# Kernel tuning notes

Hardware: AMD Instinct MI355X
Metric: run time of the kernel (lower is better)

The kernel has to match this reference:

```python
import jax, jax.numpy as jnp
import numpy as np

HIDDEN = 2048
INPUT = 128
BATCH = 2048


def setup_inputs() -> dict:
    key = jax.random.key(0)
    k = jax.random.split(key, 7)
    inp = {
        "input": jax.random.normal(k[0], (BATCH, INPUT), dtype=jnp.float32),
        "hx_real": jax.random.normal(k[1], (BATCH, HIDDEN), dtype=jnp.float32),
        "hx_imag": jax.random.normal(k[2], (BATCH, HIDDEN), dtype=jnp.float32),
        "W_unitary": jax.random.normal(k[3], (5 * HIDDEN, INPUT), dtype=jnp.float32) / np.sqrt(INPUT),
        "b_unitary": jax.random.normal(k[4], (5 * HIDDEN,), dtype=jnp.float32) * 0.01,
        "beta": jnp.zeros((HIDDEN,), dtype=jnp.float32),
        "permutation": jax.random.permutation(k[5], HIDDEN).astype(jnp.int32),
    }
    return inp


def _householder_apply(v, h):
    # (I - 2 v v^H) h = h - 2 v (v^H h); same math as materializing the matrix.
    proj = jnp.sum(jnp.conj(v) * h, axis=-1, keepdims=True)
    return h - 2.0 * v * proj


def reference(input, hx_real, hx_imag, W_unitary, b_unitary, beta, permutation):
    hx = hx_real + 1j * hx_imag  # (B, H) complex64
    up = input @ W_unitary.T + b_unitary  # (B, 5H)
    phases = jnp.exp(1j * up)  # complex64, unit modulus
    d1, d2, d3, r1, r2 = jnp.split(phases, 5, axis=-1)

    h = jnp.fft.fft(d1 * hx, axis=-1)
    h = _householder_apply(r1, h)
    h = jnp.fft.ifft(d2 * h[:, permutation], axis=-1)
    h = d3 * _householder_apply(r2, h)

    # ModReLU: relu(|z| + beta) * exp(1j * angle(z))
    mag = jnp.abs(h)
    new_mag = jax.nn.relu(mag + beta)
    h = new_mag * jnp.exp(1j * jnp.angle(h))
    return h
```

## Files before the change

kernel.cpp:

```cpp
#include <hip/hip_runtime.h>
#include <hip/hip_fp16.h>

#define HID 2048
#define FIVEH 10240
#define INP 128
#define BATCH 2048

typedef _Float16 half8 __attribute__((ext_vector_type(8)));
typedef float f32x4 __attribute__((ext_vector_type(4)));

__device__ __forceinline__ half8 cvt8(const float* p) {
  float4 a = *(const float4*)p;
  float4 b = *(const float4*)(p + 4);
  half8 h;
  h[0] = (_Float16)a.x; h[1] = (_Float16)a.y; h[2] = (_Float16)a.z; h[3] = (_Float16)a.w;
  h[4] = (_Float16)b.x; h[5] = (_Float16)b.y; h[6] = (_Float16)b.z; h[7] = (_Float16)b.w;
  return h;
}

#define WSTRIDE 136
__global__ __launch_bounds__(256) void gemm_up(const float* __restrict__ A,
                                               const float* __restrict__ W,
                                               const float* __restrict__ bias,
                                               _Float16* __restrict__ up16,
                                               int row0, int nrows) {
  __shared__ _Float16 Ws[128 * WSTRIDE];
  int tid = threadIdx.x, wave = tid >> 6, lane = tid & 63;
  int bx = blockIdx.x;
  int by = blockIdx.y;
  int nl = lane & 15, quad = lane >> 4;

  {
    const float* src = W + (size_t)(bx * 128) * INP;
#pragma unroll
    for (int it = 0; it < 8; ++it) {
      int n = (it * 256 + tid) * 8;
      int col = n >> 7, k = n & 127;
      *(half8*)(Ws + col * WSTRIDE + k) = cvt8(src + n);
    }
  }

  half8 af[2][4];
  int rowbase = row0 + by * 128 + wave * 32;
#pragma unroll
  for (int mt = 0; mt < 2; ++mt) {
    const float* ar = A + (size_t)(rowbase + mt * 16 + nl) * INP + quad * 8;
#pragma unroll
    for (int ks = 0; ks < 4; ++ks) af[mt][ks] = cvt8(ar + ks * 32);
  }
  __syncthreads();

  f32x4 acc[2][8];
#pragma unroll
  for (int nt = 0; nt < 8; ++nt) {
    half8 bf[4];
#pragma unroll
    for (int ks = 0; ks < 4; ++ks)
      bf[ks] = *(const half8*)(Ws + (nt * 16 + nl) * WSTRIDE + quad * 8 + ks * 32);
#pragma unroll
    for (int mt = 0; mt < 2; ++mt) {
      f32x4 a = {0.f, 0.f, 0.f, 0.f};
#pragma unroll
      for (int ks = 0; ks < 4; ++ks)
        a = __builtin_amdgcn_mfma_f32_16x16x32_f16(af[mt][ks], bf[ks], a, 0, 0, 0);
      acc[mt][nt] = a;
    }
  }
  __syncthreads();

#pragma unroll
  for (int nt = 0; nt < 8; ++nt) {
    float bv = bias[bx * 128 + nt * 16 + nl];
#pragma unroll
    for (int mt = 0; mt < 2; ++mt) {
      int rl = wave * 32 + mt * 16 + quad * 4;
#pragma unroll
      for (int r = 0; r < 4; ++r)
        Ws[(rl + r) * WSTRIDE + nt * 16 + nl] = (_Float16)(acc[mt][nt][r] + bv);
    }
  }
  __syncthreads();

#pragma unroll
  for (int it = 0; it < 8; ++it) {
    int v = it * 256 + tid;
    int r = v >> 4, c8 = (v & 15) * 8;
    *(half8*)(up16 + (size_t)(by * 128 + r) * FIVEH + bx * 128 + c8) =
        *(const half8*)(Ws + r * WSTRIDE + c8);
  }
}

__device__ __forceinline__ float2 h2ld(const __half2* p, int i) {
  return __half22float2(p[i]);
}
__device__ __forceinline__ void h2st(__half2* p, int i, float x, float y) {
  p[i] = __floats2half2_rn(x, y);
}

__device__ __forceinline__ void fft_head(const float2 v[8], __half2* dst, int tid, float sgn) {
  const float R2 = 0.70710678118654752f;
  float2 o[8];
  {
    float x0r = v[0].x + v[4].x, x0i = v[0].y + v[4].y;
    float x1r = v[1].x + v[5].x, x1i = v[1].y + v[5].y;
    float x2r = v[2].x + v[6].x, x2i = v[2].y + v[6].y;
    float x3r = v[3].x + v[7].x, x3i = v[3].y + v[7].y;
    float t0r = x0r + x2r, t0i = x0i + x2i, t1r = x0r - x2r, t1i = x0i - x2i;
    float t2r = x1r + x3r, t2i = x1i + x3i, t3r = x1r - x3r, t3i = x1i - x3i;
    o[0].x = t0r + t2r;       o[0].y = t0i + t2i;
    o[4].x = t0r - t2r;       o[4].y = t0i - t2i;
    o[2].x = t1r - sgn * t3i; o[2].y = t1i + sgn * t3r;
    o[6].x = t1r + sgn * t3i; o[6].y = t1i - sgn * t3r;
  }
  {
    float x0r = v[0].x - v[4].x, x0i = v[0].y - v[4].y;
    float x1r = v[1].x - v[5].x, x1i = v[1].y - v[5].y;
    float x2r = v[2].x - v[6].x, x2i = v[2].y - v[6].y;
    float x3r = v[3].x - v[7].x, x3i = v[3].y - v[7].y;
    float y1r = (x1r - sgn * x1i) * R2,  y1i = (sgn * x1r + x1i) * R2;
    float y2r = -sgn * x2i,              y2i = sgn * x2r;
    float y3r = -(x3r + sgn * x3i) * R2, y3i = (sgn * x3r - x3i) * R2;
    float t0r = x0r + y2r, t0i = x0i + y2i, t1r = x0r - y2r, t1i = x0i - y2i;
    float t2r = y1r + y3r, t2i = y1i + y3i, t3r = y1r - y3r, t3i = y1i - y3i;
    o[1].x = t0r + t2r;       o[1].y = t0i + t2i;
    o[5].x = t0r - t2r;       o[5].y = t0i - t2i;
    o[3].x = t1r - sgn * t3i; o[3].y = t1i + sgn * t3r;
    o[7].x = t1r + sgn * t3i; o[7].y = t1i - sgn * t3r;
  }
  __half2* base = dst + 8 * tid;
#pragma unroll
  for (int j = 0; j < 8; ++j) h2st(base, j, o[j].x, o[j].y);
}

template <int L>
__device__ __forceinline__ void fft_mid(const __half2* __restrict__ src,
                                        __half2* __restrict__ dst, int tid, float sgn) {
  static_assert(256 % L == 0, "twiddle hoist requires 256 % L == 0");
  const int k = tid & (L - 1);
  float s1, c1;
  __sincosf(sgn * (1.5707963267948966f / (float)L) * (float)k, &s1, &c1);
  float c2 = c1 * c1 - s1 * s1, s2 = 2.f * c1 * s1;
  float c3 = c1 * c2 - s1 * s2, s3 = c1 * s2 + s1 * c2;
#pragma unroll
  for (int t = 0; t < 2; ++t) {
    int i = tid + (t << 8);
    int base4 = ((i - k) << 2) + k;
    float2 x0 = h2ld(src, i),        x1 = h2ld(src, i + 512);
    float2 x2 = h2ld(src, i + 1024), x3 = h2ld(src, i + 1536);
    float y1r = x1.x * c1 - x1.y * s1, y1i = x1.x * s1 + x1.y * c1;
    float y2r = x2.x * c2 - x2.y * s2, y2i = x2.x * s2 + x2.y * c2;
    float y3r = x3.x * c3 - x3.y * s3, y3i = x3.x * s3 + x3.y * c3;
    float t0r = x0.x + y2r, t0i = x0.y + y2i;
    float t1r = x0.x - y2r, t1i = x0.y - y2i;
    float t2r = y1r + y3r, t2i = y1i + y3i;
    float t3r = y1r - y3r, t3i = y1i - y3i;
    h2st(dst, base4,         t0r + t2r, t0i + t2i);
    h2st(dst, base4 + 2 * L, t0r - t2r, t0i - t2i);
    h2st(dst, base4 + L,     t1r - sgn * t3i, t1i + sgn * t3r);
    h2st(dst, base4 + 3 * L, t1r + sgn * t3i, t1i - sgn * t3r);
  }
}

__device__ __forceinline__ void fft_tail(const __half2* __restrict__ src, float2 h[8],
                                         int tid, float sgn) {
#pragma unroll
  for (int t = 0; t < 2; ++t) {
    int i = tid + (t << 8);
    float s1, c1;
    __sincosf(sgn * (1.5707963267948966f / 512.f) * (float)i, &s1, &c1);
    float c2 = c1 * c1 - s1 * s1, s2 = 2.f * c1 * s1;
    float c3 = c1 * c2 - s1 * s2, s3 = c1 * s2 + s1 * c2;
    float2 x0 = h2ld(src, i),        x1 = h2ld(src, i + 512);
    float2 x2 = h2ld(src, i + 1024), x3 = h2ld(src, i + 1536);
    float y1r = x1.x * c1 - x1.y * s1, y1i = x1.x * s1 + x1.y * c1;
    float y2r = x2.x * c2 - x2.y * s2, y2i = x2.x * s2 + x2.y * c2;
    float y3r = x3.x * c3 - x3.y * s3, y3i = x3.x * s3 + x3.y * c3;
    float t0r = x0.x + y2r, t0i = x0.y + y2i;
    float t1r = x0.x - y2r, t1i = x0.y - y2i;
    float t2r = y1r + y3r, t2i = y1i + y3i;
    float t3r = y1r - y3r, t3i = y1i - y3i;
    h[t].x     = t0r + t2r;       h[t].y     = t0i + t2i;
    h[t + 4].x = t0r - t2r;       h[t + 4].y = t0i - t2i;
    h[t + 2].x = t1r - sgn * t3i; h[t + 2].y = t1i + sgn * t3r;
    h[t + 6].x = t1r + sgn * t3i; h[t + 6].y = t1i - sgn * t3r;
  }
}

__device__ __forceinline__ void block_reduce2(float& pr, float& pi,
                                              float* redr, float* redi, int tid) {
  for (int off = 32; off > 0; off >>= 1) {
    pr += __shfl_down(pr, off, 64);
    pi += __shfl_down(pi, off, 64);
  }
  if ((tid & 63) == 0) { redr[tid >> 6] = pr; redi[tid >> 6] = pi; }
  __syncthreads();
  pr = redr[0] + redr[1] + redr[2] + redr[3];
  pi = redi[0] + redi[1] + redi[2] + redi[3];
}

#define ROW_PIPELINE(UP)                                                        \
  float2 hreg[8];                                                               \
  {                                                                             \
    float2 v[8];                                                                \
    _Pragma("unroll") for (int e = 0; e < 8; ++e) {                             \
      int k = tid + (e << 8);                                                   \
      float sv, cv; __sincosf(UP(e, 0), &sv, &cv);                              \
      float hr = hxr[(size_t)b * HID + k];                                      \
      float hi = hxi[(size_t)b * HID + k];                                      \
      v[e].x = cv * hr - sv * hi; v[e].y = cv * hi + sv * hr;                   \
    }                                                                           \
    fft_head(v, sA, tid, -1.f);                                                 \
  }                                                                             \
  __syncthreads();                                                              \
  fft_mid<8>(sA, sB, tid, -1.f);   __syncthreads();                             \
  fft_mid<32>(sB, sA, tid, -1.f);  __syncthreads();                             \
  fft_mid<128>(sA, sB, tid, -1.f); __syncthreads();                             \
  fft_tail(sB, hreg, tid, -1.f);                                                \
  float cc[8], ss[8];                                                           \
  {                                                                             \
    float pr = 0.f, pi = 0.f;                                                   \
    _Pragma("unroll") for (int e = 0; e < 8; ++e) {                             \
      float sv, cv; __sincosf(UP(e, 3), &sv, &cv);                              \
      cc[e] = cv; ss[e] = sv;                                                   \
      pr += cv * hreg[e].x + sv * hreg[e].y;                                    \
      pi += cv * hreg[e].y - sv * hreg[e].x;                                    \
    }                                                                           \
    block_reduce2(pr, pi, redr, redi, tid);                                     \
    _Pragma("unroll") for (int e = 0; e < 8; ++e) {                             \
      int k = tid + (e << 8);                                                   \
      h2st(sA, k, hreg[e].x - 2.f * (cc[e] * pr - ss[e] * pi),                  \
                  hreg[e].y - 2.f * (cc[e] * pi + ss[e] * pr));                 \
    }                                                                           \
  }                                                                             \
  __syncthreads();                                                              \
  {                                                                             \
    const float invN = 1.0f / (float)HID;                                       \
    float2 v[8];                                                                \
    _Pragma("unroll") for (int e = 0; e < 8; ++e) {                             \
      int k = tid + (e << 8);                                                   \
      float sv, cv; __sincosf(UP(e, 1), &sv, &cv);                              \
      float2 hh = h2ld(sA, perm[k]);                                            \
      v[e].x = (cv * hh.x - sv * hh.y) * invN;                                  \
      v[e].y = (cv * hh.y + sv * hh.x) * invN;                                  \
    }                                                                           \
    fft_head(v, sB, tid, 1.f);                                                  \
  }                                                                             \
  __syncthreads();                                                              \
  fft_mid<8>(sB, sA, tid, 1.f);   __syncthreads();                              \
  fft_mid<32>(sA, sB, tid, 1.f);  __syncthreads();                              \
  fft_mid<128>(sB, sA, tid, 1.f); __syncthreads();                              \
  fft_tail(sA, hreg, tid, 1.f);                                                 \
  float prj_r, prj_i;                                                           \
  {                                                                             \
    float pr = 0.f, pi = 0.f;                                                   \
    _Pragma("unroll") for (int e = 0; e < 8; ++e) {                             \
      float sv, cv; __sincosf(UP(e, 4), &sv, &cv);                              \
      cc[e] = cv; ss[e] = sv;                                                   \
      pr += cv * hreg[e].x + sv * hreg[e].y;                                    \
      pi += cv * hreg[e].y - sv * hreg[e].x;                                    \
    }                                                                           \
    block_reduce2(pr, pi, redr + 4, redi + 4, tid);                             \
    prj_r = pr; prj_i = pi;                                                     \
  }                                                                             \
  _Pragma("unroll") for (int e = 0; e < 8; ++e) {                               \
    int k = tid + (e << 8);                                                     \
    float hr = hreg[e].x - 2.f * (cc[e] * prj_r - ss[e] * prj_i);               \
    float hi = hreg[e].y - 2.f * (cc[e] * prj_i + ss[e] * prj_r);               \
    float s3, c3; __sincosf(UP(e, 2), &s3, &c3);                                \
    float zr = c3 * hr - s3 * hi;                                               \
    float zi = c3 * hi + s3 * hr;                                               \
    float mag = sqrtf(zr * zr + zi * zi);                                       \
    float nm = mag + beta[k];                                                   \
    nm = nm > 0.f ? nm : 0.f;                                                   \
    float orr, oii;                                                             \
    if (mag > 0.f) { float sc = nm / mag; orr = zr * sc; oii = zi * sc; }       \
    else { orr = nm; oii = 0.f; }                                               \
    long m = (long)b * HID + k;                                                 \
    if (omode == 1) {                                                           \
      const long half = (long)BATCH * HID;                                      \
      if (half + m < out_size_l) { out[m] = orr; out[half + m] = oii; }         \
    } else if (omode == 0) {                                                    \
      if (2 * m + 1 < out_size_l) {                                             \
        float2 o; o.x = orr; o.y = oii;                                         \
        *(float2*)(out + 2 * m) = o;                                            \
      }                                                                         \
    } else {                                                                    \
      if (m < out_size_l) out[m] = orr;                                         \
    }                                                                           \
  }

__global__ __launch_bounds__(256, 4) void urnn_row(const _Float16* __restrict__ up16,
                                                   const float* __restrict__ hxr,
                                                   const float* __restrict__ hxi,
                                                   const float* __restrict__ beta,
                                                   const int* __restrict__ perm,
                                                   float* __restrict__ out,
                                                   int row0, long out_size_l, int omode) {
  __shared__ __half2 sA[HID], sB[HID];
  __shared__ float redr[8], redi[8];

  int tid = threadIdx.x;
  int b = row0 + blockIdx.x;
  const _Float16* uprow = up16 + (size_t)blockIdx.x * FIVEH;
#define UPG(e, s) ((float)uprow[(s) * HID + tid + ((e) << 8)])
  ROW_PIPELINE(UPG)
#undef UPG
}

__global__ __launch_bounds__(256) void urnn_fused(const float* __restrict__ A,
                                                  const float* __restrict__ W,
                                                  const float* __restrict__ bias,
                                                  const float* __restrict__ hxr,
                                                  const float* __restrict__ hxi,
                                                  const float* __restrict__ beta,
                                                  const int* __restrict__ perm,
                                                  float* __restrict__ out,
                                                  long out_size_l, int omode) {
  __shared__ __half2 sA[HID], sB[HID];
  __shared__ float redr[8], redi[8];
  __shared__ float4 xs4[INP / 4];

  int tid = threadIdx.x;
  int b = blockIdx.x;

  if (tid < INP / 4) xs4[tid] = ((const float4*)(A + (size_t)b * INP))[tid];
  __syncthreads();

  float upreg[40];
#pragma unroll
  for (int se = 0; se < 40; ++se) {
    int n = ((se >> 3) << 11) + ((se & 7) << 8) + tid;
    upreg[se] = bias[n];
  }
  for (int kb = 0; kb < 4; ++kb) {
    float4 xv[8];
#pragma unroll
    for (int j = 0; j < 8; ++j) xv[j] = xs4[kb * 8 + j];
#pragma unroll
    for (int se = 0; se < 40; ++se) {
      int n = ((se >> 3) << 11) + ((se & 7) << 8) + tid;
      const float4* wr = (const float4*)(W + (size_t)n * INP + (kb << 5));
      float a = 0.f;
#pragma unroll
      for (int j = 0; j < 8; ++j) {
        float4 wv = wr[j];
        a += xv[j].x * wv.x + xv[j].y * wv.y + xv[j].z * wv.z + xv[j].w * wv.w;
      }
      upreg[se] += a;
    }
  }
#define UPR(e, s) (upreg[(s) * 8 + (e)])
  ROW_PIPELINE(UPR)
#undef UPR
}

extern "C" void kernel_launch(void* const* d_in, const int* in_sizes, int n_in,
                              void* d_out, int out_size, void* d_ws, size_t ws_size,
                              hipStream_t stream) {
  const float* input   = (const float*)d_in[0];
  const float* hx_real = (const float*)d_in[1];
  const float* hx_imag = (const float*)d_in[2];
  const float* W       = (const float*)d_in[3];
  const float* bvec    = (const float*)d_in[4];
  const float* beta    = (const float*)d_in[5];
  const int*   perm    = (const int*)d_in[6];

  int omode;
  if (out_size == BATCH * HID) omode = 2;
  else if (out_size == 2 * BATCH * HID) omode = 1;
  else omode = 0;

  const size_t rowbytes = (size_t)FIVEH * sizeof(_Float16);
  long chunk = (long)(ws_size / rowbytes);
  if (chunk > BATCH) chunk = BATCH;
  chunk &= ~127L;

  if (chunk >= 128) {
    _Float16* up16 = (_Float16*)d_ws;
    for (long row0 = 0; row0 < BATCH; row0 += chunk) {
      int rows = (int)((row0 + chunk <= BATCH) ? chunk : (BATCH - row0));
      dim3 g(FIVEH / 128, rows / 128);
      gemm_up<<<g, 256, 0, stream>>>(input, W, bvec, up16, (int)row0, rows);
      urnn_row<<<rows, 256, 0, stream>>>(up16, hx_real, hx_imag, beta, perm,
                                         (float*)d_out, (int)row0, (long)out_size, omode);
    }
  } else {
    urnn_fused<<<BATCH, 256, 0, stream>>>(input, W, bvec, hx_real, hx_imag, beta, perm,
                                          (float*)d_out, (long)out_size, omode);
  }
}
```

Measured before the change: 144.4 us.

## Process two batch rows per block in the per-row FFT kernel

Replaces the one-row-per-block urnn_row kernel with urnn_row2, which handles two rows per 256-thread block using doubled shared buffers. FFT twiddle factors, the permutation indices and the tail twiddles are computed once per block and reused across both rows, and the two rows share barriers. This cuts redundant sincos and sync overhead per row, at the cost of twice the shared memory per block, a lower occupancy hint (launch bounds 2 instead of 4), and half as many blocks.

```diff
diff --git a/kernel.cpp b/kernel.cpp
--- a/kernel.cpp
+++ b/kernel.cpp
@@ -161,20 +161,64 @@
   }
 }
 
-__device__ __forceinline__ void fft_tail(const __half2* __restrict__ src, float2 h[8],
+template <int L>
+__device__ __forceinline__ void fft_mid2(const __half2 (*__restrict__ src)[HID],
+                                         __half2 (*__restrict__ dst)[HID],
                                          int tid, float sgn) {
+  static_assert(256 % L == 0, "twiddle hoist requires 256 % L == 0");
+  const int k = tid & (L - 1);
+  float s1, c1;
+  __sincosf(sgn * (1.5707963267948966f / (float)L) * (float)k, &s1, &c1);
+  float c2 = c1 * c1 - s1 * s1, s2 = 2.f * c1 * s1;
+  float c3 = c1 * c2 - s1 * s2, s3 = c1 * s2 + s1 * c2;
+#pragma unroll
+  for (int r = 0; r < 2; ++r) {
+#pragma unroll
+    for (int t = 0; t < 2; ++t) {
+      int i = tid + (t << 8);
+      int base4 = ((i - k) << 2) + k;
+      float2 x0 = h2ld(src[r], i),        x1 = h2ld(src[r], i + 512);
+      float2 x2 = h2ld(src[r], i + 1024), x3 = h2ld(src[r], i + 1536);
+      float y1r = x1.x * c1 - x1.y * s1, y1i = x1.x * s1 + x1.y * c1;
+      float y2r = x2.x * c2 - x2.y * s2, y2i = x2.x * s2 + x2.y * c2;
+      float y3r = x3.x * c3 - x3.y * s3, y3i = x3.x * s3 + x3.y * c3;
+      float t0r = x0.x + y2r, t0i = x0.y + y2i;
+      float t1r = x0.x - y2r, t1i = x0.y - y2i;
+      float t2r = y1r + y3r, t2i = y1i + y3i;
+      float t3r = y1r - y3r, t3i = y1i - y3i;
+      h2st(dst[r], base4,         t0r + t2r, t0i + t2i);
+      h2st(dst[r], base4 + 2 * L, t0r - t2r, t0i - t2i);
+      h2st(dst[r], base4 + L,     t1r - sgn * t3i, t1i + sgn * t3r);
+      h2st(dst[r], base4 + 3 * L, t1r + sgn * t3i, t1i - sgn * t3r);
+    }
+  }
+}
+
+struct TailTw { float c1[2], s1[2], c2[2], s2[2], c3[2], s3[2]; };
+__device__ __forceinline__ TailTw tail_tw(int tid, float sgn) {
+  TailTw w;
 #pragma unroll
   for (int t = 0; t < 2; ++t) {
     int i = tid + (t << 8);
     float s1, c1;
     __sincosf(sgn * (1.5707963267948966f / 512.f) * (float)i, &s1, &c1);
-    float c2 = c1 * c1 - s1 * s1, s2 = 2.f * c1 * s1;
-    float c3 = c1 * c2 - s1 * s2, s3 = c1 * s2 + s1 * c2;
+    w.c1[t] = c1; w.s1[t] = s1;
+    w.c2[t] = c1 * c1 - s1 * s1; w.s2[t] = 2.f * c1 * s1;
+    w.c3[t] = c1 * w.c2[t] - s1 * w.s2[t]; w.s3[t] = c1 * w.s2[t] + s1 * w.c2[t];
+  }
+  return w;
+}
+
+__device__ __forceinline__ void fft_tail_row(const __half2* __restrict__ src, float2 h[8],
+                                             int tid, float sgn, const TailTw& w) {
+#pragma unroll
+  for (int t = 0; t < 2; ++t) {
+    int i = tid + (t << 8);
     float2 x0 = h2ld(src, i),        x1 = h2ld(src, i + 512);
     float2 x2 = h2ld(src, i + 1024), x3 = h2ld(src, i + 1536);
-    float y1r = x1.x * c1 - x1.y * s1, y1i = x1.x * s1 + x1.y * c1;
-    float y2r = x2.x * c2 - x2.y * s2, y2i = x2.x * s2 + x2.y * c2;
-    float y3r = x3.x * c3 - x3.y * s3, y3i = x3.x * s3 + x3.y * c3;
+    float y1r = x1.x * w.c1[t] - x1.y * w.s1[t], y1i = x1.x * w.s1[t] + x1.y * w.c1[t];
+    float y2r = x2.x * w.c2[t] - x2.y * w.s2[t], y2i = x2.x * w.s2[t] + x2.y * w.c2[t];
+    float y3r = x3.x * w.c3[t] - x3.y * w.s3[t], y3i = x3.x * w.s3[t] + x3.y * w.c3[t];
     float t0r = x0.x + y2r, t0i = x0.y + y2i;
     float t1r = x0.x - y2r, t1i = x0.y - y2i;
     float t2r = y1r + y3r, t2i = y1i + y3i;
@@ -186,6 +230,12 @@
   }
 }
 
+__device__ __forceinline__ void fft_tail(const __half2* __restrict__ src, float2 h[8],
+                                         int tid, float sgn) {
+  TailTw w = tail_tw(tid, sgn);
+  fft_tail_row(src, h, tid, sgn, w);
+}
+
 __device__ __forceinline__ void block_reduce2(float& pr, float& pi,
                                               float* redr, float* redi, int tid) {
   for (int off = 32; off > 0; off >>= 1) {
@@ -196,6 +246,141 @@
   __syncthreads();
   pr = redr[0] + redr[1] + redr[2] + redr[3];
   pi = redi[0] + redi[1] + redi[2] + redi[3];
+}
+
+__global__ __launch_bounds__(256, 2) void urnn_row2(const _Float16* __restrict__ up16,
+                                                    const float* __restrict__ hxr,
+                                                    const float* __restrict__ hxi,
+                                                    const float* __restrict__ beta,
+                                                    const int* __restrict__ perm,
+                                                    float* __restrict__ out,
+                                                    int row0, long out_size_l, int omode) {
+  __shared__ __half2 sA[2][HID], sB[2][HID];
+  __shared__ float redr[16], redi[16];
+
+  int tid = threadIdx.x;
+  int rb = blockIdx.x * 2;
+  int b0 = row0 + rb;
+  const _Float16* up0 = up16 + (size_t)rb * FIVEH;
+
+#pragma unroll
+  for (int r = 0; r < 2; ++r) {
+    const _Float16* up = up0 + (size_t)r * FIVEH;
+    float2 v[8];
+#pragma unroll
+    for (int e = 0; e < 8; ++e) {
+      int k = tid + (e << 8);
+      float sv, cv; __sincosf((float)up[k], &sv, &cv);
+      float hr = hxr[(size_t)(b0 + r) * HID + k];
+      float hi = hxi[(size_t)(b0 + r) * HID + k];
+      v[e].x = cv * hr - sv * hi; v[e].y = cv * hi + sv * hr;
+    }
+    fft_head(v, sA[r], tid, -1.f);
+  }
+  __syncthreads();
+  fft_mid2<8>(sA, sB, tid, -1.f);   __syncthreads();
+  fft_mid2<32>(sB, sA, tid, -1.f);  __syncthreads();
+  fft_mid2<128>(sA, sB, tid, -1.f); __syncthreads();
+
+  {
+    TailTw w = tail_tw(tid, -1.f);
+#pragma unroll
+    for (int r = 0; r < 2; ++r) {
+      const _Float16* up = up0 + (size_t)r * FIVEH;
+      float2 hreg[8];
+      fft_tail_row(sB[r], hreg, tid, -1.f, w);
+      float cc[8], ss[8];
+      float pr = 0.f, pi = 0.f;
+#pragma unroll
+      for (int e = 0; e < 8; ++e) {
+        float sv, cv; __sincosf((float)up[3 * HID + tid + (e << 8)], &sv, &cv);
+        cc[e] = cv; ss[e] = sv;
+        pr += cv * hreg[e].x + sv * hreg[e].y;
+        pi += cv * hreg[e].y - sv * hreg[e].x;
+      }
+      block_reduce2(pr, pi, redr + 4 * r, redi + 4 * r, tid);
+#pragma unroll
+      for (int e = 0; e < 8; ++e) {
+        int k = tid + (e << 8);
+        h2st(sA[r], k, hreg[e].x - 2.f * (cc[e] * pr - ss[e] * pi),
+                       hreg[e].y - 2.f * (cc[e] * pi + ss[e] * pr));
+      }
+    }
+  }
+  __syncthreads();
+
+  {
+    int pk[8];
+#pragma unroll
+    for (int e = 0; e < 8; ++e) pk[e] = perm[tid + (e << 8)];
+    const float invN = 1.0f / (float)HID;
+#pragma unroll
+    for (int r = 0; r < 2; ++r) {
+      const _Float16* up = up0 + (size_t)r * FIVEH;
+      float2 v[8];
+#pragma unroll
+      for (int e = 0; e < 8; ++e) {
+        int k = tid + (e << 8);
+        float sv, cv; __sincosf((float)up[HID + k], &sv, &cv);
+        float2 hh = h2ld(sA[r], pk[e]);
+        v[e].x = (cv * hh.x - sv * hh.y) * invN;
+        v[e].y = (cv * hh.y + sv * hh.x) * invN;
+      }
+      fft_head(v, sB[r], tid, 1.f);
+    }
+  }
+  __syncthreads();
+  fft_mid2<8>(sB, sA, tid, 1.f);   __syncthreads();
+  fft_mid2<32>(sA, sB, tid, 1.f);  __syncthreads();
+  fft_mid2<128>(sB, sA, tid, 1.f); __syncthreads();
+
+  {
+    TailTw w = tail_tw(tid, 1.f);
+#pragma unroll
+    for (int r = 0; r < 2; ++r) {
+      const _Float16* up = up0 + (size_t)r * FIVEH;
+      long b = b0 + r;
+      float2 hreg[8];
+      fft_tail_row(sA[r], hreg, tid, 1.f, w);
+      float cc[8], ss[8];
+      float pr = 0.f, pi = 0.f;
+#pragma unroll
+      for (int e = 0; e < 8; ++e) {
+        float sv, cv; __sincosf((float)up[4 * HID + tid + (e << 8)], &sv, &cv);
+        cc[e] = cv; ss[e] = sv;
+        pr += cv * hreg[e].x + sv * hreg[e].y;
+        pi += cv * hreg[e].y - sv * hreg[e].x;
+      }
+      block_reduce2(pr, pi, redr + 8 + 4 * r, redi + 8 + 4 * r, tid);
+#pragma unroll
+      for (int e = 0; e < 8; ++e) {
+        int k = tid + (e << 8);
+        float hr = hreg[e].x - 2.f * (cc[e] * pr - ss[e] * pi);
+        float hi = hreg[e].y - 2.f * (cc[e] * pi + ss[e] * pr);
+        float s3, c3; __sincosf((float)up[2 * HID + k], &s3, &c3);
+        float zr = c3 * hr - s3 * hi;
+        float zi = c3 * hi + s3 * hr;
+        float mag = sqrtf(zr * zr + zi * zi);
+        float nm = mag + beta[k];
+        nm = nm > 0.f ? nm : 0.f;
+        float orr, oii;
+        if (mag > 0.f) { float sc = nm / mag; orr = zr * sc; oii = zi * sc; }
+        else { orr = nm; oii = 0.f; }
+        long m = b * HID + k;
+        if (omode == 1) {
+          const long half = (long)BATCH * HID;
+          if (half + m < out_size_l) { out[m] = orr; out[half + m] = oii; }
+        } else if (omode == 0) {
+          if (2 * m + 1 < out_size_l) {
+            float2 o; o.x = orr; o.y = oii;
+            *(float2*)(out + 2 * m) = o;
+          }
+        } else {
+          if (m < out_size_l) out[m] = orr;
+        }
+      }
+    }
+  }
 }
 
 #define ROW_PIPELINE(UP)                                                        \
@@ -289,24 +474,6 @@
     }                                                                           \
   }
 
-__global__ __launch_bounds__(256, 4) void urnn_row(const _Float16* __restrict__ up16,
-                                                   const float* __restrict__ hxr,
-                                                   const float* __restrict__ hxi,
-                                                   const float* __restrict__ beta,
-                                                   const int* __restrict__ perm,
-                                                   float* __restrict__ out,
-                                                   int row0, long out_size_l, int omode) {
-  __shared__ __half2 sA[HID], sB[HID];
-  __shared__ float redr[8], redi[8];
-
-  int tid = threadIdx.x;
-  int b = row0 + blockIdx.x;
-  const _Float16* uprow = up16 + (size_t)blockIdx.x * FIVEH;
-#define UPG(e, s) ((float)uprow[(s) * HID + tid + ((e) << 8)])
-  ROW_PIPELINE(UPG)
-#undef UPG
-}
-
 __global__ __launch_bounds__(256) void urnn_fused(const float* __restrict__ A,
                                                   const float* __restrict__ W,
                                                   const float* __restrict__ bias,
@@ -381,8 +548,8 @@
       int rows = (int)((row0 + chunk <= BATCH) ? chunk : (BATCH - row0));
       dim3 g(FIVEH / 128, rows / 128);
       gemm_up<<<g, 256, 0, stream>>>(input, W, bvec, up16, (int)row0, rows);
-      urnn_row<<<rows, 256, 0, stream>>>(up16, hx_real, hx_imag, beta, perm,
-                                         (float*)d_out, (int)row0, (long)out_size, omode);
+      urnn_row2<<<rows / 2, 256, 0, stream>>>(up16, hx_real, hx_imag, beta, perm,
+                                              (float*)d_out, (int)row0, (long)out_size, omode);
     }
   } else {
     urnn_fused<<<BATCH, 256, 0, stream>>>(input, W, bvec, hx_real, hx_imag, beta, perm,
```

New measurement: 152.6 us. 1.06x slower.

## Restructure FFT as radix-8 passes with fp32 shared-memory staging

Applied to the files above, without the earlier changes.

Replaces the radix-8 head plus three radix-4 middle passes with a radix-8 head, two radix-8 passes and the radix-4 tail, cutting the number of shared-memory round trips and barriers per FFT. Shared-memory buffers change from half2 to float2, which removes the fp16 conversions and improves accuracy. In exchange it doubles shared-memory use per block, which may reduce occupancy, and the radix-8 passes use more registers for twiddles.

```diff
diff --git a/kernel.cpp b/kernel.cpp
--- a/kernel.cpp
+++ b/kernel.cpp
@@ -90,79 +90,79 @@
   }
 }
 
-__device__ __forceinline__ float2 h2ld(const __half2* p, int i) {
-  return __half22float2(p[i]);
-}
-__device__ __forceinline__ void h2st(__half2* p, int i, float x, float y) {
-  p[i] = __floats2half2_rn(x, y);
-}
-
-__device__ __forceinline__ void fft_head(const float2 v[8], __half2* dst, int tid, float sgn) {
+__device__ __forceinline__ float2 cmulcs(float2 a, float c, float s) {
+  float2 r; r.x = a.x * c - a.y * s; r.y = a.x * s + a.y * c; return r;
+}
+
+__device__ __forceinline__ void dft8(const float2 y[8], float2 o[8], float sgn) {
   const float R2 = 0.70710678118654752f;
+  float ta0r = y[0].x + y[4].x, ta0i = y[0].y + y[4].y;
+  float ta1r = y[0].x - y[4].x, ta1i = y[0].y - y[4].y;
+  float ta2r = y[2].x + y[6].x, ta2i = y[2].y + y[6].y;
+  float ta3r = y[2].x - y[6].x, ta3i = y[2].y - y[6].y;
+  float E0r = ta0r + ta2r, E0i = ta0i + ta2i;
+  float E2r = ta0r - ta2r, E2i = ta0i - ta2i;
+  float E1r = ta1r - sgn * ta3i, E1i = ta1i + sgn * ta3r;
+  float E3r = ta1r + sgn * ta3i, E3i = ta1i - sgn * ta3r;
+  float tb0r = y[1].x + y[5].x, tb0i = y[1].y + y[5].y;
+  float tb1r = y[1].x - y[5].x, tb1i = y[1].y - y[5].y;
+  float tb2r = y[3].x + y[7].x, tb2i = y[3].y + y[7].y;
+  float tb3r = y[3].x - y[7].x, tb3i = y[3].y - y[7].y;
+  float O0r = tb0r + tb2r, O0i = tb0i + tb2i;
+  float O2r = tb0r - tb2r, O2i = tb0i - tb2i;
+  float O1r = tb1r - sgn * tb3i, O1i = tb1i + sgn * tb3r;
+  float O3r = tb1r + sgn * tb3i, O3i = tb1i - sgn * tb3r;
+  float p1r = R2 * (O1r - sgn * O1i), p1i = R2 * (O1i + sgn * O1r);
+  float p2r = -sgn * O2i,             p2i = sgn * O2r;
+  float p3r = -R2 * (O3r + sgn * O3i), p3i = R2 * (sgn * O3r - O3i);
+  o[0].x = E0r + O0r; o[0].y = E0i + O0i;
+  o[4].x = E0r - O0r; o[4].y = E0i - O0i;
+  o[1].x = E1r + p1r; o[1].y = E1i + p1i;
+  o[5].x = E1r - p1r; o[5].y = E1i - p1i;
+  o[2].x = E2r + p2r; o[2].y = E2i + p2i;
+  o[6].x = E2r - p2r; o[6].y = E2i - p2i;
+  o[3].x = E3r + p3r; o[3].y = E3i + p3i;
+  o[7].x = E3r - p3r; o[7].y = E3i - p3i;
+}
+
+__device__ __forceinline__ void fft8_head(const float2 v[8], float2* dst, int tid, float sgn) {
   float2 o[8];
-  {
-    float x0r = v[0].x + v[4].x, x0i = v[0].y + v[4].y;
-    float x1r = v[1].x + v[5].x, x1i = v[1].y + v[5].y;
-    float x2r = v[2].x + v[6].x, x2i = v[2].y + v[6].y;
-    float x3r = v[3].x + v[7].x, x3i = v[3].y + v[7].y;
-    float t0r = x0r + x2r, t0i = x0i + x2i, t1r = x0r - x2r, t1i = x0i - x2i;
-    float t2r = x1r + x3r, t2i = x1i + x3i, t3r = x1r - x3r, t3i = x1i - x3i;
-    o[0].x = t0r + t2r;       o[0].y = t0i + t2i;
-    o[4].x = t0r - t2r;       o[4].y = t0i - t2i;
-    o[2].x = t1r - sgn * t3i; o[2].y = t1i + sgn * t3r;
-    o[6].x = t1r + sgn * t3i; o[6].y = t1i - sgn * t3r;
-  }
-  {
-    float x0r = v[0].x - v[4].x, x0i = v[0].y - v[4].y;
-    float x1r = v[1].x - v[5].x, x1i = v[1].y - v[5].y;
-    float x2r = v[2].x - v[6].x, x2i = v[2].y - v[6].y;
-    float x3r = v[3].x - v[7].x, x3i = v[3].y - v[7].y;
-    float y1r = (x1r - sgn * x1i) * R2,  y1i = (sgn * x1r + x1i) * R2;
-    float y2r = -sgn * x2i,              y2i = sgn * x2r;
-    float y3r = -(x3r + sgn * x3i) * R2, y3i = (sgn * x3r - x3i) * R2;
-    float t0r = x0r + y2r, t0i = x0i + y2i, t1r = x0r - y2r, t1i = x0i - y2i;
-    float t2r = y1r + y3r, t2i = y1i + y3i, t3r = y1r - y3r, t3i = y1i - y3i;
-    o[1].x = t0r + t2r;       o[1].y = t0i + t2i;
-    o[5].x = t0r - t2r;       o[5].y = t0i - t2i;
-    o[3].x = t1r - sgn * t3i; o[3].y = t1i + sgn * t3r;
-    o[7].x = t1r + sgn * t3i; o[7].y = t1i - sgn * t3r;
-  }
-  __half2* base = dst + 8 * tid;
-#pragma unroll
-  for (int j = 0; j < 8; ++j) h2st(base, j, o[j].x, o[j].y);
+  dft8(v, o, sgn);
+  float2* base = dst + (tid << 3);
+#pragma unroll
+  for (int j = 0; j < 8; ++j) base[j] = o[j];
 }
 
 template <int L>
-__device__ __forceinline__ void fft_mid(const __half2* __restrict__ src,
-                                        __half2* __restrict__ dst, int tid, float sgn) {
-  static_assert(256 % L == 0, "twiddle hoist requires 256 % L == 0");
+__device__ __forceinline__ void fft8_pass(const float2* __restrict__ src,
+                                          float2* __restrict__ dst, int tid, float sgn) {
   const int k = tid & (L - 1);
   float s1, c1;
-  __sincosf(sgn * (1.5707963267948966f / (float)L) * (float)k, &s1, &c1);
-  float c2 = c1 * c1 - s1 * s1, s2 = 2.f * c1 * s1;
-  float c3 = c1 * c2 - s1 * s2, s3 = c1 * s2 + s1 * c2;
-#pragma unroll
-  for (int t = 0; t < 2; ++t) {
-    int i = tid + (t << 8);
-    int base4 = ((i - k) << 2) + k;
-    float2 x0 = h2ld(src, i),        x1 = h2ld(src, i + 512);
-    float2 x2 = h2ld(src, i + 1024), x3 = h2ld(src, i + 1536);
-    float y1r = x1.x * c1 - x1.y * s1, y1i = x1.x * s1 + x1.y * c1;
-    float y2r = x2.x * c2 - x2.y * s2, y2i = x2.x * s2 + x2.y * c2;
-    float y3r = x3.x * c3 - x3.y * s3, y3i = x3.x * s3 + x3.y * c3;
-    float t0r = x0.x + y2r, t0i = x0.y + y2i;
-    float t1r = x0.x - y2r, t1i = x0.y - y2i;
-    float t2r = y1r + y3r, t2i = y1i + y3i;
-    float t3r = y1r - y3r, t3i = y1i - y3i;
-    h2st(dst, base4,         t0r + t2r, t0i + t2i);
-    h2st(dst, base4 + 2 * L, t0r - t2r, t0i - t2i);
-    h2st(dst, base4 + L,     t1r - sgn * t3i, t1i + sgn * t3r);
-    h2st(dst, base4 + 3 * L, t1r + sgn * t3i, t1i - sgn * t3r);
-  }
-}
-
-__device__ __forceinline__ void fft_tail(const __half2* __restrict__ src, float2 h[8],
-                                         int tid, float sgn) {
+  __sincosf(sgn * (0.78539816339744831f / (float)L) * (float)k, &s1, &c1);
+  float c2 = c1 * c1 - s1 * s1,  s2 = 2.f * c1 * s1;
+  float c3 = c2 * c1 - s2 * s1,  s3 = c2 * s1 + s2 * c1;
+  float c4 = c2 * c2 - s2 * s2,  s4 = 2.f * c2 * s2;
+  float c5 = c4 * c1 - s4 * s1,  s5 = c4 * s1 + s4 * c1;
+  float c6 = c4 * c2 - s4 * s2,  s6 = c4 * s2 + s4 * c2;
+  float c7 = c4 * c3 - s4 * s3,  s7 = c4 * s3 + s4 * c3;
+  float2 y[8];
+  y[0] = src[tid];
+  y[1] = cmulcs(src[tid + 256],  c1, s1);
+  y[2] = cmulcs(src[tid + 512],  c2, s2);
+  y[3] = cmulcs(src[tid + 768],  c3, s3);
+  y[4] = cmulcs(src[tid + 1024], c4, s4);
+  y[5] = cmulcs(src[tid + 1280], c5, s5);
+  y[6] = cmulcs(src[tid + 1536], c6, s6);
+  y[7] = cmulcs(src[tid + 1792], c7, s7);
+  float2 o[8];
+  dft8(y, o, sgn);
+  const int base = ((tid - k) << 3) + k;
+#pragma unroll
+  for (int j = 0; j < 8; ++j) dst[base + j * L] = o[j];
+}
+
+__device__ __forceinline__ void fft_tail_f(const float2* __restrict__ src, float2 h[8],
+                                           int tid, float sgn) {
 #pragma unroll
   for (int t = 0; t < 2; ++t) {
     int i = tid + (t << 8);
@@ -170,8 +170,7 @@
     __sincosf(sgn * (1.5707963267948966f / 512.f) * (float)i, &s1, &c1);
     float c2 = c1 * c1 - s1 * s1, s2 = 2.f * c1 * s1;
     float c3 = c1 * c2 - s1 * s2, s3 = c1 * s2 + s1 * c2;
-    float2 x0 = h2ld(src, i),        x1 = h2ld(src, i + 512);
-    float2 x2 = h2ld(src, i + 1024), x3 = h2ld(src, i + 1536);
+    float2 x0 = src[i], x1 = src[i + 512], x2 = src[i + 1024], x3 = src[i + 1536];
     float y1r = x1.x * c1 - x1.y * s1, y1i = x1.x * s1 + x1.y * c1;
     float y2r = x2.x * c2 - x2.y * s2, y2i = x2.x * s2 + x2.y * c2;
     float y3r = x3.x * c3 - x3.y * s3, y3i = x3.x * s3 + x3.y * c3;
@@ -209,13 +208,12 @@
       float hi = hxi[(size_t)b * HID + k];                                      \
       v[e].x = cv * hr - sv * hi; v[e].y = cv * hi + sv * hr;                   \
     }                                                                           \
-    fft_head(v, sA, tid, -1.f);                                                 \
+    fft8_head(v, sA, tid, -1.f);                                                \
   }                                                                             \
   __syncthreads();                                                              \
-  fft_mid<8>(sA, sB, tid, -1.f);   __syncthreads();                             \
-  fft_mid<32>(sB, sA, tid, -1.f);  __syncthreads();                             \
-  fft_mid<128>(sA, sB, tid, -1.f); __syncthreads();                             \
-  fft_tail(sB, hreg, tid, -1.f);                                                \
+  fft8_pass<8>(sA, sB, tid, -1.f);  __syncthreads();                            \
+  fft8_pass<64>(sB, sA, tid, -1.f); __syncthreads();                            \
+  fft_tail_f(sA, hreg, tid, -1.f);                                              \
   float cc[8], ss[8];                                                           \
   {                                                                             \
     float pr = 0.f, pi = 0.f;                                                   \
@@ -228,8 +226,8 @@
     block_reduce2(pr, pi, redr, redi, tid);                                     \
     _Pragma("unroll") for (int e = 0; e < 8; ++e) {                             \
       int k = tid + (e << 8);                                                   \
-      h2st(sA, k, hreg[e].x - 2.f * (cc[e] * pr - ss[e] * pi),                  \
-                  hreg[e].y - 2.f * (cc[e] * pi + ss[e] * pr));                 \
+      sB[k].x = hreg[e].x - 2.f * (cc[e] * pr - ss[e] * pi);                    \
+      sB[k].y = hreg[e].y - 2.f * (cc[e] * pi + ss[e] * pr);                    \
     }                                                                           \
   }                                                                             \
   __syncthreads();                                                              \
@@ -239,17 +237,16 @@
     _Pragma("unroll") for (int e = 0; e < 8; ++e) {                             \
       int k = tid + (e << 8);                                                   \
       float sv, cv; __sincosf(UP(e, 1), &sv, &cv);                              \
-      float2 hh = h2ld(sA, perm[k]);                                            \
+      float2 hh = sB[perm[k]];                                                  \
       v[e].x = (cv * hh.x - sv * hh.y) * invN;                                  \
       v[e].y = (cv * hh.y + sv * hh.x) * invN;                                  \
     }                                                                           \
-    fft_head(v, sB, tid, 1.f);                                                  \
+    fft8_head(v, sA, tid, 1.f);                                                 \
   }                                                                             \
   __syncthreads();                                                              \
-  fft_mid<8>(sB, sA, tid, 1.f);   __syncthreads();                              \
-  fft_mid<32>(sA, sB, tid, 1.f);  __syncthreads();                              \
-  fft_mid<128>(sB, sA, tid, 1.f); __syncthreads();                              \
-  fft_tail(sA, hreg, tid, 1.f);                                                 \
+  fft8_pass<8>(sA, sB, tid, 1.f);  __syncthreads();                             \
+  fft8_pass<64>(sB, sA, tid, 1.f); __syncthreads();                             \
+  fft_tail_f(sA, hreg, tid, 1.f);                                               \
   float prj_r, prj_i;                                                           \
   {                                                                             \
     float pr = 0.f, pi = 0.f;                                                   \
@@ -296,7 +293,7 @@
                                                    const int* __restrict__ perm,
                                                    float* __restrict__ out,
                                                    int row0, long out_size_l, int omode) {
-  __shared__ __half2 sA[HID], sB[HID];
+  __shared__ float2 sA[HID], sB[HID];
   __shared__ float redr[8], redi[8];
 
   int tid = threadIdx.x;
@@ -316,7 +313,7 @@
                                                   const int* __restrict__ perm,
                                                   float* __restrict__ out,
                                                   long out_size_l, int omode) {
-  __shared__ __half2 sA[HID], sB[HID];
+  __shared__ float2 sA[HID], sB[HID];
   __shared__ float redr[8], redi[8];
   __shared__ float4 xs4[INP / 4];
 
```

Measured after the change: 145.6 us. Within noise of the previous version (+0.8%).
